# Kernel tuning notes

Hardware: AMD Instinct MI355X
Metric: run time of the kernel (lower is better)

## Reference

```python
import jax, jax.numpy as jnp
import numpy as np

SEQ, B, IN, H = 512, 64, 1024, 1024


def setup_inputs() -> dict:
    key = jax.random.key(0)
    k0, k1, k2, k3, k4 = jax.random.split(key, 5)
    stdv = 1.0 / np.sqrt(H)
    Xt = jax.random.normal(k0, (SEQ, B, IN), dtype=jnp.float32)
    # layer 0: concat(x[IN], h0[H]) -> H ; layer 1: concat(y0[H], h1[H]) -> H
    W0 = jax.random.uniform(k1, (H, IN + H), dtype=jnp.float32, minval=-stdv, maxval=stdv)
    b0 = jax.random.uniform(k2, (H,), dtype=jnp.float32, minval=-stdv, maxval=stdv)
    W1 = jax.random.uniform(k3, (H, H + H), dtype=jnp.float32, minval=-stdv, maxval=stdv)
    b1 = jax.random.uniform(k4, (H,), dtype=jnp.float32, minval=-stdv, maxval=stdv)
    return {"Xt": Xt, "W0": W0, "b0": b0, "W1": W1, "b1": b1}


def reference(Xt, W0, b0, W1, b1):
    # Concatenated-gate stacked tanh RNN (n_states=1), seq-major layout [S,B,F].
    Bsz = Xt.shape[1]
    h0 = jnp.zeros((Bsz, W0.shape[0]), dtype=Xt.dtype)
    h1 = jnp.zeros((Bsz, W1.shape[0]), dtype=Xt.dtype)

    def step(carry, x):
        h0, h1 = carry
        h0n = jnp.tanh(jnp.concatenate([x, h0], axis=-1) @ W0.T + b0)
        h1n = jnp.tanh(jnp.concatenate([h0n, h1], axis=-1) @ W1.T + b1)
        return (h0n, h1n), h1n

    (_, _), Y = jax.lax.scan(step, (h0, h1), Xt)
    return Y  # [SEQ, B, H] — stacked top-layer outputs (stack_output=True)
```

## Files before the change

### kernel.cpp

```cpp
#include <hip/hip_runtime.h>


typedef unsigned short ushort_t;
typedef unsigned int uint32;
typedef __attribute__((ext_vector_type(2))) unsigned int u32x2;
typedef __attribute__((ext_vector_type(4))) unsigned int u32x4;
typedef __attribute__((ext_vector_type(2))) float f32x2;
typedef __attribute__((ext_vector_type(4))) float f32x4;
typedef __attribute__((ext_vector_type(8))) __bf16 bfrag;

__device__ __forceinline__ uint32 bf16rne(float f) {
  uint32 u = __builtin_bit_cast(uint32, f);
  return (u + 0x7fffu + ((u >> 16) & 1u)) >> 16;
}

__device__ __forceinline__ f32x4 mfma_bf16(u32x4 a, u32x4 b, f32x4 c) {
  return __builtin_amdgcn_mfma_f32_16x16x32_bf16(
      __builtin_bit_cast(bfrag, a), __builtin_bit_cast(bfrag, b), c, 0, 0, 0);
}

__device__ __forceinline__ void spin_ge(const int* p, int tgt) {
  int v;
  do {
    asm volatile("global_load_dword %0, %1, off sc0 sc1\n\ts_waitcnt vmcnt(0)"
                 : "=v"(v) : "v"(p) : "memory");
  } while (v < tgt);
}

__device__ __forceinline__ void load_sc16(u32x4 (&dst)[16], const ushort_t* base) {
#pragma unroll
  for (int kk = 0; kk < 16; ++kk)
    asm volatile("global_load_dwordx4 %0, %1, off sc0 sc1"
                 : "=v"(dst[kk]) : "v"(base + 32 * kk) : "memory");
}

__global__ __launch_bounds__(256) void rnn_prep(
    const float* __restrict__ Xt, const float* __restrict__ W0,
    const float* __restrict__ W1, ushort_t* __restrict__ Xbf,
    ushort_t* __restrict__ W0bf, ushort_t* __restrict__ W1bf,
    int* __restrict__ flags) {
  const long nX = 512L * 64 * 1024 / 4;
  const long nW = 1024L * 2048 / 4;
  const long total = nX + 2 * nW;
  long stride = (long)gridDim.x * blockDim.x;
  for (long v = (long)blockIdx.x * blockDim.x + threadIdx.x; v < total; v += stride) {
    const float* src;
    ushort_t* dst;
    long off;
    if (v < nX) { src = Xt; dst = Xbf; off = v; }
    else if (v < nX + nW) { src = W0; dst = W0bf; off = v - nX; }
    else { src = W1; dst = W1bf; off = v - nX - nW; }
    f32x4 f = *(const f32x4*)(src + off * 4);
    u32x2 o;
    o.x = bf16rne(f.x) | (bf16rne(f.y) << 16);
    o.y = bf16rne(f.z) | (bf16rne(f.w) << 16);
    *(u32x2*)(dst + off * 4) = o;
  }
  int t0 = blockIdx.x * blockDim.x + threadIdx.x;
  if (t0 < 128) {
    int z = 0;
    asm volatile("global_store_dword %0, %1, off sc0 sc1\n\ts_waitcnt vmcnt(0)"
                 :: "v"(flags + t0), "v"(z) : "memory");
  }
}

__global__ __launch_bounds__(512) void rnn_main(
    const ushort_t* __restrict__ Xbf,
    const ushort_t* __restrict__ W0bf,
    const ushort_t* __restrict__ W1bf,
    const float* __restrict__ b0, const float* __restrict__ b1,
    ushort_t* h0buf,
    ushort_t* h1buf,
    float* __restrict__ Y,
    int* flag0, int* flag1) {
  __shared__ float part[8][32][20];

  const int tid = threadIdx.x;
  const int wave = tid >> 6;
  const int lane = tid & 63;
  const int ln15 = lane & 15;
  const int lq = lane >> 4;
  const int kq = wave & 3;
  const int mh = wave >> 2;
  const int g = blockIdx.x;
  const bool isL1 = (g >= 64);
  const int gl = isL1 ? g - 64 : g;
  const int F0 = gl * 16;
  const int koff = (kq & 1) * 512;
  const int mt0 = mh * 2;
  const bool hcons = (kq >= 2);

  const ushort_t* Wsrc = isL1 ? W1bf : W0bf;
  u32x4 bw[16];
  {
    const ushort_t* wp = Wsrc + (size_t)(F0 + ln15) * 2048 + kq * 512 + lq * 8;
#pragma unroll
    for (int kk = 0; kk < 16; ++kk) bw[kk] = *(const u32x4*)(wp + kk * 32);
  }

  const int rm = tid >> 3;
  const int rml = rm & 31;
  const int rmh4 = (rm >> 5) * 4;
  const int rf = (tid & 7) * 2;
  const float* bsrc = isL1 ? b1 : b0;
  const float bia0 = bsrc[F0 + rf];
  const float bia1 = bsrc[F0 + rf + 1];

  for (int t = 0; t < 512; ++t) {
    if (!isL1) {
      if (hcons) { if (t >= 1) spin_ge(flag0 + lane, t); }
      else if (wave == 0 && t >= 2) spin_ge(flag1 + lane, t - 1);
    } else {
      if (!hcons) spin_ge(flag0 + lane, t + 1);
      else if (t >= 1) spin_ge(flag1 + lane, t);
    }

    f32x4 aA0 = {0.f, 0.f, 0.f, 0.f}, aB0 = aA0, aA1 = aA0, aB1 = aA0;
    const bool active = (t >= 1) || !hcons;
    if (active) {
      if (!isL1 && !hcons) {
        const ushort_t* ax = Xbf + (size_t)t * 65536 + koff + lq * 8;
        const ushort_t* p0 = ax + (size_t)(mt0 * 16 + ln15) * 1024;
        const ushort_t* p1 = p0 + 16 * 1024;
#pragma unroll
        for (int kk = 0; kk < 16; ++kk) {
          u32x4 a0 = *(const u32x4*)(p0 + kk * 32);
          u32x4 a1 = *(const u32x4*)(p1 + kk * 32);
          if (kk & 1) { aB0 = mfma_bf16(a0, bw[kk], aB0); aB1 = mfma_bf16(a1, bw[kk], aB1); }
          else        { aA0 = mfma_bf16(a0, bw[kk], aA0); aA1 = mfma_bf16(a1, bw[kk], aA1); }
        }
      } else {
        const ushort_t* hb;
        if (!isL1)       hb = h0buf + ((t - 1) & 1) * 65536;
        else if (!hcons) hb = h0buf + (t & 1) * 65536;
        else             hb = h1buf + ((t - 1) & 1) * 65536;
        const ushort_t* p0 = hb + (size_t)(mt0 * 16 + ln15) * 1024 + koff + lq * 8;
        const ushort_t* p1 = p0 + 16 * 1024;
        u32x4 fA[16], fB[16];
        load_sc16(fA, p0);
        load_sc16(fB, p1);
        asm volatile("s_waitcnt vmcnt(0)" ::: "memory");
        __builtin_amdgcn_sched_barrier(0);
#pragma unroll
        for (int kk = 0; kk < 16; ++kk) {
          if (kk & 1) { aB0 = mfma_bf16(fA[kk], bw[kk], aB0); aB1 = mfma_bf16(fB[kk], bw[kk], aB1); }
          else        { aA0 = mfma_bf16(fA[kk], bw[kk], aA0); aA1 = mfma_bf16(fB[kk], bw[kk], aA1); }
        }
      }
    }

    {
      f32x4 s0 = aA0 + aB0, s1 = aA1 + aB1;
#pragma unroll
      for (int r = 0; r < 4; ++r) {
        part[wave][lq * 4 + r][ln15] = s0[r];
        part[wave][16 + lq * 4 + r][ln15] = s1[r];
      }
    }
    __syncthreads();

    {
      float s0 = 0.f, s1 = 0.f;
#pragma unroll
      for (int w = 0; w < 4; ++w) {
        f32x2 v = *(const f32x2*)&part[rmh4 + w][rml][rf];
        s0 += v.x; s1 += v.y;
      }
      float y0 = tanhf(s0 + bia0);
      float y1 = tanhf(s1 + bia1);
      uint32 hp = bf16rne(y0) | (bf16rne(y1) << 16);
      ushort_t* hd = (isL1 ? h1buf : h0buf) + (t & 1) * 65536 + rm * 1024 + F0 + rf;
      asm volatile("global_store_dword %0, %1, off sc0 sc1" :: "v"(hd), "v"(hp) : "memory");
      if (isL1) {
        f32x2 yv = {y0, y1};
        *(f32x2*)(Y + ((size_t)t * 64 + rm) * 1024 + F0 + rf) = yv;
      }
      asm volatile("s_waitcnt vmcnt(0)" ::: "memory");
    }
    __syncthreads();
    if (tid == 0) {
      int* fp = (isL1 ? flag1 : flag0) + gl;
      int val = t + 1;
      asm volatile("global_store_dword %0, %1, off sc0 sc1\n\ts_waitcnt vmcnt(0)"
                   :: "v"(fp), "v"(val) : "memory");
    }
  }
}

extern "C" void kernel_launch(void* const* d_in, const int* in_sizes, int n_in,
                              void* d_out, int out_size, void* d_ws, size_t ws_size,
                              hipStream_t stream) {
  const float* Xt = (const float*)d_in[0];
  const float* W0 = (const float*)d_in[1];
  const float* b0 = (const float*)d_in[2];
  const float* W1 = (const float*)d_in[3];
  const float* b1 = (const float*)d_in[4];
  float* Y = (float*)d_out;

  ushort_t* Xbf = (ushort_t*)d_ws;
  ushort_t* W0bf = Xbf + (size_t)512 * 64 * 1024;
  ushort_t* W1bf = W0bf + (size_t)1024 * 2048;
  ushort_t* h0buf = W1bf + (size_t)1024 * 2048;
  ushort_t* h1buf = h0buf + (size_t)2 * 64 * 1024;
  int* flags = (int*)(h1buf + (size_t)2 * 64 * 1024);

  rnn_prep<<<2048, 256, 0, stream>>>(Xt, W0, W1, Xbf, W0bf, W1bf, flags);
  rnn_main<<<128, 512, 0, stream>>>(Xbf, W0bf, W1bf, b0, b1, h0buf, h1buf, Y,
                                    flags, flags + 64);
}
```

Baseline: 5.305 ms.

## Partition batch across XCDs with per-XCD counters and fused bf16 conversion

Replaces the two-kernel design with an init kernel plus a 256-block main kernel. Blocks read their XCC_ID and take slots through an atomic, so each XCD independently runs the full two-layer recurrence for 8 batch rows. Hidden-state traffic and synchronisation counters stay local to one XCD's L2, and per-block flags become atomic counters. Weights and inputs are converted to bf16 in-kernel, removing the separate prep pass. It also adds a fast tanh, pipelined h loads and an abort/timeout escape in the spin loop, but relies on exactly 32 blocks landing on each XCD, which is a scheduling assumption.

```diff
diff --git a/kernel.cpp b/kernel.cpp
--- a/kernel.cpp
+++ b/kernel.cpp
@@ -3,186 +3,240 @@
 
 typedef unsigned short ushort_t;
 typedef unsigned int uint32;
-typedef __attribute__((ext_vector_type(2))) unsigned int u32x2;
 typedef __attribute__((ext_vector_type(4))) unsigned int u32x4;
-typedef __attribute__((ext_vector_type(2))) float f32x2;
 typedef __attribute__((ext_vector_type(4))) float f32x4;
 typedef __attribute__((ext_vector_type(8))) __bf16 bfrag;
+
+__device__ __forceinline__ f32x4 mfma_bf16(u32x4 a, u32x4 b, f32x4 c) {
+  return __builtin_amdgcn_mfma_f32_16x16x32_bf16(
+      __builtin_bit_cast(bfrag, a), __builtin_bit_cast(bfrag, b), c, 0, 0, 0);
+}
 
 __device__ __forceinline__ uint32 bf16rne(float f) {
   uint32 u = __builtin_bit_cast(uint32, f);
   return (u + 0x7fffu + ((u >> 16) & 1u)) >> 16;
 }
 
-__device__ __forceinline__ f32x4 mfma_bf16(u32x4 a, u32x4 b, f32x4 c) {
-  return __builtin_amdgcn_mfma_f32_16x16x32_bf16(
-      __builtin_bit_cast(bfrag, a), __builtin_bit_cast(bfrag, b), c, 0, 0, 0);
-}
-
-__device__ __forceinline__ void spin_ge(const int* p, int tgt) {
-  int v;
-  do {
+__device__ __forceinline__ uint32 cvt_pk(float lo, float hi) {
+  uint32 r;
+  asm("v_cvt_pk_bf16_f32 %0, %1, %2" : "=v"(r) : "v"(lo), "v"(hi));
+  return r;
+}
+__device__ __forceinline__ u32x4 pack8(f32x4 a, f32x4 b) {
+  u32x4 r;
+  r.x = cvt_pk(a.x, a.y);
+  r.y = cvt_pk(a.z, a.w);
+  r.z = cvt_pk(b.x, b.y);
+  r.w = cvt_pk(b.z, b.w);
+  return r;
+}
+
+template <int BOFF>
+__device__ __forceinline__ void ld16(u32x4& d, const ushort_t* base) {
+  asm volatile("global_load_dwordx4 %0, %1, off offset:%c2 sc0"
+               : "=v"(d) : "v"(base), "i"(BOFF) : "memory");
+}
+
+#define LOADB(BUF, AP, KOFF)                 \
+  ld16<(KOFF) * 2 + 0>(BUF[0], AP);          \
+  ld16<(KOFF) * 2 + 64>(BUF[1], AP);         \
+  ld16<(KOFF) * 2 + 128>(BUF[2], AP);        \
+  ld16<(KOFF) * 2 + 192>(BUF[3], AP);        \
+  ld16<(KOFF) * 2 + 256>(BUF[4], AP);        \
+  ld16<(KOFF) * 2 + 320>(BUF[5], AP);        \
+  ld16<(KOFF) * 2 + 384>(BUF[6], AP);        \
+  ld16<(KOFF) * 2 + 448>(BUF[7], AP);
+
+__device__ __forceinline__ void spin_ctr(const int* p, int tgt, int* ab) {
+  int it = 0;
+  for (;;) {
+    int v;
     asm volatile("global_load_dword %0, %1, off sc0 sc1\n\ts_waitcnt vmcnt(0)"
                  : "=v"(v) : "v"(p) : "memory");
-  } while (v < tgt);
-}
-
-__device__ __forceinline__ void load_sc16(u32x4 (&dst)[16], const ushort_t* base) {
-#pragma unroll
-  for (int kk = 0; kk < 16; ++kk)
-    asm volatile("global_load_dwordx4 %0, %1, off sc0 sc1"
-                 : "=v"(dst[kk]) : "v"(base + 32 * kk) : "memory");
-}
-
-__global__ __launch_bounds__(256) void rnn_prep(
+    if (v >= tgt) return;
+    if ((++it & 1023) == 0) {
+      int a;
+      asm volatile("global_load_dword %0, %1, off sc0 sc1\n\ts_waitcnt vmcnt(0)"
+                   : "=v"(a) : "v"(ab) : "memory");
+      if (a) return;
+      if (it > (1 << 21)) {
+        int one = 1;
+        asm volatile("global_store_dword %0, %1, off sc0 sc1\n\ts_waitcnt vmcnt(0)"
+                     :: "v"(ab), "v"(one) : "memory");
+        return;
+      }
+    }
+  }
+}
+
+__global__ void rnn_init(int* c) {
+  for (int k = threadIdx.x; k < 772; k += 256) {
+    int z = 0;
+    asm volatile("global_store_dword %0, %1, off sc0 sc1"
+                 :: "v"(c + k), "v"(z) : "memory");
+  }
+  asm volatile("s_waitcnt vmcnt(0)" ::: "memory");
+}
+
+__global__ __launch_bounds__(512, 2) void rnn_main(
     const float* __restrict__ Xt, const float* __restrict__ W0,
-    const float* __restrict__ W1, ushort_t* __restrict__ Xbf,
-    ushort_t* __restrict__ W0bf, ushort_t* __restrict__ W1bf,
-    int* __restrict__ flags) {
-  const long nX = 512L * 64 * 1024 / 4;
-  const long nW = 1024L * 2048 / 4;
-  const long total = nX + 2 * nW;
-  long stride = (long)gridDim.x * blockDim.x;
-  for (long v = (long)blockIdx.x * blockDim.x + threadIdx.x; v < total; v += stride) {
-    const float* src;
-    ushort_t* dst;
-    long off;
-    if (v < nX) { src = Xt; dst = Xbf; off = v; }
-    else if (v < nX + nW) { src = W0; dst = W0bf; off = v - nX; }
-    else { src = W1; dst = W1bf; off = v - nX - nW; }
-    f32x4 f = *(const f32x4*)(src + off * 4);
-    u32x2 o;
-    o.x = bf16rne(f.x) | (bf16rne(f.y) << 16);
-    o.y = bf16rne(f.z) | (bf16rne(f.w) << 16);
-    *(u32x2*)(dst + off * 4) = o;
-  }
-  int t0 = blockIdx.x * blockDim.x + threadIdx.x;
-  if (t0 < 128) {
-    int z = 0;
-    asm volatile("global_store_dword %0, %1, off sc0 sc1\n\ts_waitcnt vmcnt(0)"
-                 :: "v"(flags + t0), "v"(z) : "memory");
-  }
-}
-
-__global__ __launch_bounds__(512) void rnn_main(
-    const ushort_t* __restrict__ Xbf,
-    const ushort_t* __restrict__ W0bf,
-    const ushort_t* __restrict__ W1bf,
-    const float* __restrict__ b0, const float* __restrict__ b1,
-    ushort_t* h0buf,
-    ushort_t* h1buf,
-    float* __restrict__ Y,
-    int* flag0, int* flag1) {
-  __shared__ float part[8][32][20];
+    const float* __restrict__ b0, const float* __restrict__ W1,
+    const float* __restrict__ b1, float* __restrict__ Y,
+    ushort_t* hbuf, int* cnt) {
+  __shared__ float part[2][4][16][17];
+  __shared__ int s_slot;
 
   const int tid = threadIdx.x;
   const int wave = tid >> 6;
   const int lane = tid & 63;
   const int ln15 = lane & 15;
   const int lq = lane >> 4;
-  const int kq = wave & 3;
-  const int mh = wave >> 2;
-  const int g = blockIdx.x;
-  const bool isL1 = (g >= 64);
-  const int gl = isL1 ? g - 64 : g;
-  const int F0 = gl * 16;
-  const int koff = (kq & 1) * 512;
-  const int mt0 = mh * 2;
-  const bool hcons = (kq >= 2);
-
-  const ushort_t* Wsrc = isL1 ? W1bf : W0bf;
-  u32x4 bw[16];
+  const int n = wave & 3;
+  const bool fin = wave < 4;
+
+  uint32 xcc;
+  asm("s_getreg_b32 %0, hwreg(HW_REG_XCC_ID)" : "=s"(xcc));
+  const int xcd = xcc & 7;
+
+  int* slotp  = cnt + xcd * 96;
+  int* ctr0   = cnt + xcd * 96 + 32;
+  int* ctr1   = cnt + xcd * 96 + 64;
+  int* abortp = cnt + 768;
+
+  if (tid == 0) {
+    int one = 1, old;
+    asm volatile("global_atomic_add %0, %1, %2, off sc0 sc1\n\ts_waitcnt vmcnt(0)"
+                 : "=v"(old) : "v"(slotp), "v"(one) : "memory");
+    s_slot = old & 31;
+  }
+  __syncthreads();
+  const int slot = s_slot;
+  const bool isL1 = slot >= 16;
+  const int F0 = (slot & 15) * 64;
+  const int fcol = F0 + n * 16 + ln15;
+  const int row8 = ln15 & 7;
+
+  const int kh = isL1 ? (fin ? 0 : 1) : (fin ? 1 : 0);
+  const float* Wsrc = isL1 ? W1 : W0;
+
+  u32x4 bw[32];
   {
-    const ushort_t* wp = Wsrc + (size_t)(F0 + ln15) * 2048 + kq * 512 + lq * 8;
-#pragma unroll
-    for (int kk = 0; kk < 16; ++kk) bw[kk] = *(const u32x4*)(wp + kk * 32);
-  }
-
-  const int rm = tid >> 3;
-  const int rml = rm & 31;
-  const int rmh4 = (rm >> 5) * 4;
-  const int rf = (tid & 7) * 2;
-  const float* bsrc = isL1 ? b1 : b0;
-  const float bia0 = bsrc[F0 + rf];
-  const float bia1 = bsrc[F0 + rf + 1];
+    const float* wp = Wsrc + (size_t)fcol * 2048 + kh * 1024 + lq * 8;
+#pragma unroll 4
+    for (int j = 0; j < 32; ++j) {
+      f32x4 w0 = *(const f32x4*)(wp + j * 32);
+      f32x4 w1 = *(const f32x4*)(wp + j * 32 + 4);
+      bw[j] = pack8(w0, w1);
+    }
+  }
+  const float bia = fin ? (isL1 ? b1 : b0)[fcol] : 0.f;
+
+  ushort_t* h0b = hbuf + (size_t)xcd * 32768;
+  ushort_t* h1b = h0b + 16384;
+
+  auto gemm_h = [&](const ushort_t* hsrc) -> f32x4 {
+    f32x4 a = {0.f, 0.f, 0.f, 0.f};
+    const ushort_t* ap = hsrc + row8 * 1024 + lq * 8;
+    u32x4 fa[8], fb[8];
+    LOADB(fa, ap, 0);
+    LOADB(fb, ap, 256);
+    asm volatile("s_waitcnt vmcnt(8)" ::: "memory");
+    __builtin_amdgcn_sched_barrier(0);
+#pragma unroll
+    for (int j = 0; j < 8; ++j) a = mfma_bf16(fa[j], bw[j], a);
+    LOADB(fa, ap, 512);
+    asm volatile("s_waitcnt vmcnt(8)" ::: "memory");
+    __builtin_amdgcn_sched_barrier(0);
+#pragma unroll
+    for (int j = 0; j < 8; ++j) a = mfma_bf16(fb[j], bw[8 + j], a);
+    LOADB(fb, ap, 768);
+    asm volatile("s_waitcnt vmcnt(8)" ::: "memory");
+    __builtin_amdgcn_sched_barrier(0);
+#pragma unroll
+    for (int j = 0; j < 8; ++j) a = mfma_bf16(fa[j], bw[16 + j], a);
+    asm volatile("s_waitcnt vmcnt(0)" ::: "memory");
+    __builtin_amdgcn_sched_barrier(0);
+#pragma unroll
+    for (int j = 0; j < 8; ++j) a = mfma_bf16(fb[j], bw[24 + j], a);
+    return a;
+  };
+
+  auto gemm_x = [&](int t) -> f32x4 {
+    f32x4 a = {0.f, 0.f, 0.f, 0.f};
+    const float* xp = Xt + ((size_t)t * 64 + xcd * 8 + row8) * 1024 + lq * 8;
+#pragma unroll 4
+    for (int j = 0; j < 32; ++j) {
+      f32x4 x0 = *(const f32x4*)(xp + j * 32);
+      f32x4 x1 = *(const f32x4*)(xp + j * 32 + 4);
+      a = mfma_bf16(pack8(x0, x1), bw[j], a);
+    }
+    return a;
+  };
 
   for (int t = 0; t < 512; ++t) {
+    const int buf = t & 1;
+    const int pb = (t - 1) & 1;
+    f32x4 acc = {0.f, 0.f, 0.f, 0.f};
+
     if (!isL1) {
-      if (hcons) { if (t >= 1) spin_ge(flag0 + lane, t); }
-      else if (wave == 0 && t >= 2) spin_ge(flag1 + lane, t - 1);
+      if (fin) {
+        if (t >= 1) spin_ctr(ctr0, 16 * t, abortp);
+        if (t >= 2) spin_ctr(ctr1, 16 * (t - 1), abortp);
+        if (t >= 1) acc = gemm_h(h0b + pb * 8192);
+      } else {
+        acc = gemm_x(t);
+      }
     } else {
-      if (!hcons) spin_ge(flag0 + lane, t + 1);
-      else if (t >= 1) spin_ge(flag1 + lane, t);
-    }
-
-    f32x4 aA0 = {0.f, 0.f, 0.f, 0.f}, aB0 = aA0, aA1 = aA0, aB1 = aA0;
-    const bool active = (t >= 1) || !hcons;
-    if (active) {
-      if (!isL1 && !hcons) {
-        const ushort_t* ax = Xbf + (size_t)t * 65536 + koff + lq * 8;
-        const ushort_t* p0 = ax + (size_t)(mt0 * 16 + ln15) * 1024;
-        const ushort_t* p1 = p0 + 16 * 1024;
-#pragma unroll
-        for (int kk = 0; kk < 16; ++kk) {
-          u32x4 a0 = *(const u32x4*)(p0 + kk * 32);
-          u32x4 a1 = *(const u32x4*)(p1 + kk * 32);
-          if (kk & 1) { aB0 = mfma_bf16(a0, bw[kk], aB0); aB1 = mfma_bf16(a1, bw[kk], aB1); }
-          else        { aA0 = mfma_bf16(a0, bw[kk], aA0); aA1 = mfma_bf16(a1, bw[kk], aA1); }
+      if (fin) {
+        if (t >= 1) spin_ctr(ctr1, 16 * t, abortp);
+        spin_ctr(ctr0, 16 * (t + 1), abortp);
+        acc = gemm_h(h0b + buf * 8192);
+      } else {
+        if (t >= 1) {
+          spin_ctr(ctr1, 16 * t, abortp);
+          acc = gemm_h(h1b + pb * 8192);
         }
-      } else {
-        const ushort_t* hb;
-        if (!isL1)       hb = h0buf + ((t - 1) & 1) * 65536;
-        else if (!hcons) hb = h0buf + (t & 1) * 65536;
-        else             hb = h1buf + ((t - 1) & 1) * 65536;
-        const ushort_t* p0 = hb + (size_t)(mt0 * 16 + ln15) * 1024 + koff + lq * 8;
-        const ushort_t* p1 = p0 + 16 * 1024;
-        u32x4 fA[16], fB[16];
-        load_sc16(fA, p0);
-        load_sc16(fB, p1);
-        asm volatile("s_waitcnt vmcnt(0)" ::: "memory");
-        __builtin_amdgcn_sched_barrier(0);
-#pragma unroll
-        for (int kk = 0; kk < 16; ++kk) {
-          if (kk & 1) { aB0 = mfma_bf16(fA[kk], bw[kk], aB0); aB1 = mfma_bf16(fB[kk], bw[kk], aB1); }
-          else        { aA0 = mfma_bf16(fA[kk], bw[kk], aA0); aA1 = mfma_bf16(fB[kk], bw[kk], aA1); }
+      }
+    }
+
+    if (!fin) {
+#pragma unroll
+      for (int r = 0; r < 4; ++r) part[buf][n][lq * 4 + r][ln15] = acc[r];
+    }
+    __syncthreads();
+
+    if (fin) {
+      float o[4];
+#pragma unroll
+      for (int r = 0; r < 4; ++r) {
+        float s = acc[r] + part[buf][n][lq * 4 + r][ln15] + bia;
+        float ax = fabsf(s);
+        float e = __expf(2.f * ax);
+        float rr = 1.f - 2.f * __builtin_amdgcn_rcpf(e + 1.f);
+        o[r] = copysignf(rr, s);
+      }
+      if (lq < 2) {
+        ushort_t* hd = (isL1 ? h1b : h0b) + buf * 8192 + (lq * 4) * 1024 + fcol;
+#pragma unroll
+        for (int r = 0; r < 4; ++r) {
+          uint32 hv = bf16rne(o[r]);
+          asm volatile("global_store_short %0, %1, off sc0"
+                       :: "v"(hd + r * 1024), "v"(hv) : "memory");
         }
-      }
-    }
-
-    {
-      f32x4 s0 = aA0 + aB0, s1 = aA1 + aB1;
-#pragma unroll
-      for (int r = 0; r < 4; ++r) {
-        part[wave][lq * 4 + r][ln15] = s0[r];
-        part[wave][16 + lq * 4 + r][ln15] = s1[r];
-      }
+        if (isL1) {
+          float* yd = Y + ((size_t)t * 64 + xcd * 8 + lq * 4) * 1024 + fcol;
+#pragma unroll
+          for (int r = 0; r < 4; ++r) yd[r * 1024] = o[r];
+        }
+      }
+      asm volatile("s_waitcnt vmcnt(0)" ::: "memory");
     }
     __syncthreads();
 
-    {
-      float s0 = 0.f, s1 = 0.f;
-#pragma unroll
-      for (int w = 0; w < 4; ++w) {
-        f32x2 v = *(const f32x2*)&part[rmh4 + w][rml][rf];
-        s0 += v.x; s1 += v.y;
-      }
-      float y0 = tanhf(s0 + bia0);
-      float y1 = tanhf(s1 + bia1);
-      uint32 hp = bf16rne(y0) | (bf16rne(y1) << 16);
-      ushort_t* hd = (isL1 ? h1buf : h0buf) + (t & 1) * 65536 + rm * 1024 + F0 + rf;
-      asm volatile("global_store_dword %0, %1, off sc0 sc1" :: "v"(hd), "v"(hp) : "memory");
-      if (isL1) {
-        f32x2 yv = {y0, y1};
-        *(f32x2*)(Y + ((size_t)t * 64 + rm) * 1024 + F0 + rf) = yv;
-      }
-      asm volatile("s_waitcnt vmcnt(0)" ::: "memory");
-    }
-    __syncthreads();
     if (tid == 0) {
-      int* fp = (isL1 ? flag1 : flag0) + gl;
-      int val = t + 1;
-      asm volatile("global_store_dword %0, %1, off sc0 sc1\n\ts_waitcnt vmcnt(0)"
-                   :: "v"(fp), "v"(val) : "memory");
+      int one = 1;
+      int* cp = isL1 ? ctr1 : ctr0;
+      asm volatile("global_atomic_add %0, %1, off sc1" :: "v"(cp), "v"(one) : "memory");
     }
   }
 }
@@ -197,14 +251,9 @@
   const float* b1 = (const float*)d_in[4];
   float* Y = (float*)d_out;
 
-  ushort_t* Xbf = (ushort_t*)d_ws;
-  ushort_t* W0bf = Xbf + (size_t)512 * 64 * 1024;
-  ushort_t* W1bf = W0bf + (size_t)1024 * 2048;
-  ushort_t* h0buf = W1bf + (size_t)1024 * 2048;
-  ushort_t* h1buf = h0buf + (size_t)2 * 64 * 1024;
-  int* flags = (int*)(h1buf + (size_t)2 * 64 * 1024);
-
-  rnn_prep<<<2048, 256, 0, stream>>>(Xt, W0, W1, Xbf, W0bf, W1bf, flags);
-  rnn_main<<<128, 512, 0, stream>>>(Xbf, W0bf, W1bf, b0, b1, h0buf, h1buf, Y,
-                                    flags, flags + 64);
-}
+  int* cnt = (int*)d_ws;
+  ushort_t* hbuf = (ushort_t*)((char*)d_ws + 4096);
+
+  rnn_init<<<1, 256, 0, stream>>>(cnt);
+  rnn_main<<<256, 512, 0, stream>>>(Xt, W0, b0, W1, b1, Y, hbuf, cnt);
+}
```

Result: slower. 9.998 ms (+88.5%).
